# Optimization experiments

Measured on AMD Instinct MI355X. Metric: run time of the kernel, lower is better.

The kernel has to match this reference:

```python
import jax, jax.numpy as jnp
import numpy as np

N, FIN, F, H = 4096, 128, 64, 8
NEG = -1e10


def setup_inputs() -> dict:
    key = jax.random.key(0)
    ks = jax.random.split(key, 6)
    X = jax.random.normal(ks[0], (N, FIN), dtype=jnp.float32)
    # sparse-ish binary adjacency with self loops, stored dense (as the layer expects)
    A = (jax.random.uniform(ks[1], (N, N)) < 0.05).astype(jnp.int32)
    A = A.at[jnp.arange(N), jnp.arange(N)].set(1)
    W = jax.random.normal(ks[2], (H, FIN, F), dtype=jnp.float32) * (1.0 / np.sqrt(FIN))
    b = jnp.zeros((H, F), dtype=jnp.float32)
    a_self = jax.random.normal(ks[3], (H, F), dtype=jnp.float32) * (1.0 / np.sqrt(F))
    a_neigh = jax.random.normal(ks[4], (H, F), dtype=jnp.float32) * (1.0 / np.sqrt(F))
    return {"X": X, "A": A, "W": W, "b": b, "a_self": a_self, "a_neigh": a_neigh}


def reference(X, A, W, b, a_self, a_neigh):
    # Dropout layers run in inference mode in the original call -> identity.
    feats = jnp.einsum('nf,hfo->hno', X, W)              # [H, N, F]
    s_self = jnp.einsum('hno,ho->hn', feats, a_self)     # [H, N]
    s_neigh = jnp.einsum('hno,ho->hn', feats, a_neigh)   # [H, N]
    scores = s_self[:, :, None] + s_neigh[:, None, :]    # [H, N, N]
    scores = jnp.where(scores > 0, scores, 0.2 * scores)  # LeakyReLU(0.2)
    mask = (1.0 - A.astype(jnp.float32)) * NEG            # [N, N]
    attn = jax.nn.softmax(scores + mask[None], axis=-1)   # [H, N, N]
    out = jnp.einsum('hnm,hmo->hno', attn, feats) + b[:, None, :]
    out = jax.nn.elu(out)                                 # [H, N, F]
    # concat heads -> [N, H*F]
    return jnp.transpose(out, (1, 0, 2)).reshape(N, H * F)
```

## Files before the change

### kernel.cpp

```cpp
#include <hip/hip_runtime.h>
#include <cmath>


#define NN 4096
#define FIN 128
#define FF 64
#define HH 8

typedef _Float16 h2 __attribute__((ext_vector_type(2)));
typedef _Float16 h4 __attribute__((ext_vector_type(4)));
typedef _Float16 h8 __attribute__((ext_vector_type(8)));
typedef float f32x2 __attribute__((ext_vector_type(2)));
typedef float f32x4 __attribute__((ext_vector_type(4)));

union H8 {
  h8 v;
  h2 p[4];
};
union H4 {
  h4 v;
  h2 p[2];
};

static __device__ __forceinline__ float dot2acc(h2 a, float c) {
#if __has_builtin(__builtin_amdgcn_fdot2)
  return __builtin_amdgcn_fdot2(a, (h2){(_Float16)1.f, (_Float16)1.f}, c,
                                false);
#else
  return c + (float)a[0] + (float)a[1];
#endif
}

__global__ __launch_bounds__(256) void pack_kernel(
    const int* __restrict__ A, const float* __restrict__ W,
    unsigned long long* __restrict__ bits, _Float16* __restrict__ Wt16) {
  const int b = blockIdx.x;
  const int tid = threadIdx.x;
  if (b < NN) {
    const int wave = tid >> 6, lane = tid & 63;
    const int* ar = A + (size_t)b * NN;
#pragma unroll
    for (int g = 0; g < 4; ++g) {
      const int w0 = wave * 16 + g * 4;
      int v0 = ar[(w0 + 0) * 64 + lane];
      int v1 = ar[(w0 + 1) * 64 + lane];
      int v2 = ar[(w0 + 2) * 64 + lane];
      int v3 = ar[(w0 + 3) * 64 + lane];
      unsigned long long m0 = __ballot(v0 != 0);
      unsigned long long m1 = __ballot(v1 != 0);
      unsigned long long m2 = __ballot(v2 != 0);
      unsigned long long m3 = __ballot(v3 != 0);
      if (lane == 0) {
        bits[(b << 6) + w0 + 0] = m0;
        bits[(b << 6) + w0 + 1] = m1;
        bits[(b << 6) + w0 + 2] = m2;
        bits[(b << 6) + w0 + 3] = m3;
      }
    }
  } else {
    const int h0 = (b - NN) * 4;
    for (int h = h0; h < h0 + 4; ++h) {
      for (int idx = tid; idx < FIN * (FF / 4); idx += 256) {
        int k = idx >> 4, f4 = (idx & 15) << 2;
        f32x4 w = *(const f32x4*)(W + ((size_t)(h * FIN + k)) * FF + f4);
#pragma unroll
        for (int j = 0; j < 4; ++j)
          Wt16[((size_t)(h * FF + f4 + j)) * FIN + k] = (_Float16)w[j];
      }
    }
  }
}

__global__ __launch_bounds__(256) void feats_kernel(
    const float* __restrict__ X, const _Float16* __restrict__ Wt16,
    const float* __restrict__ a_self, const float* __restrict__ a_neigh,
    _Float16* __restrict__ feats_sw, _Float16* __restrict__ es_h,
    _Float16* __restrict__ esn_h, _Float16* __restrict__ et_h,
    _Float16* __restrict__ etn_h) {
  const int h = blockIdx.y;
  const int tid = threadIdx.x, wave = tid >> 6, lane = tid & 63;
  const int l16 = lane & 15, quad = lane >> 4;
  const int r0 = blockIdx.x * 64 + wave * 16;

  f32x4 acc[4];
#pragma unroll
  for (int nb = 0; nb < 4; ++nb) acc[nb] = (f32x4){0.f, 0.f, 0.f, 0.f};

  const float* xr = X + (size_t)(r0 + l16) * FIN;
  const _Float16* wb = Wt16 + (size_t)h * FF * FIN;
#pragma unroll
  for (int kt = 0; kt < 4; ++kt) {
    const int kof = kt * 32 + quad * 8;
    f32x4 x0 = *(const f32x4*)(xr + kof);
    f32x4 x1 = *(const f32x4*)(xr + kof + 4);
    h8 Af = {(_Float16)x0[0], (_Float16)x0[1], (_Float16)x0[2],
             (_Float16)x0[3], (_Float16)x1[0], (_Float16)x1[1],
             (_Float16)x1[2], (_Float16)x1[3]};
#pragma unroll
    for (int nb = 0; nb < 4; ++nb) {
      h8 Bf = *(const h8*)(wb + (size_t)(nb * 16 + l16) * FIN + kof);
      acc[nb] = __builtin_amdgcn_mfma_f32_16x16x32_f16(Af, Bf, acc[nb], 0, 0, 0);
    }
  }

  float as[4], an[4];
#pragma unroll
  for (int nb = 0; nb < 4; ++nb) {
    as[nb] = a_self[h * FF + nb * 16 + l16];
    an[nb] = a_neigh[h * FF + nb * 16 + l16];
  }
#pragma unroll
  for (int r = 0; r < 4; ++r) {
    float ps = acc[0][r] * as[0] + acc[1][r] * as[1] + acc[2][r] * as[2] +
               acc[3][r] * as[3];
    float pn = acc[0][r] * an[0] + acc[1][r] * an[1] + acc[2][r] * an[2] +
               acc[3][r] * an[3];
#pragma unroll
    for (int m = 1; m <= 8; m <<= 1) {
      ps += __shfl_xor(ps, m, 64);
      pn += __shfl_xor(pn, m, 64);
    }
    if (l16 == 0) {
      int node = h * NN + r0 + quad * 4 + r;
      es_h[node] = (_Float16)__expf(ps - 2.0f);
      esn_h[node] = (_Float16)__expf(0.2f * ps - 2.0f);
      et_h[node] = (_Float16)__expf(pn - 2.0f);
      etn_h[node] = (_Float16)__expf(0.2f * pn - 2.0f);
    }
  }

  const int kb = r0 >> 5;
  const int quadA = ((r0 >> 4) & 1) * 2 + (quad >> 1);
  const int jbase = (quad & 1) << 2;
#pragma unroll
  for (int nb = 0; nb < 4; ++nb) {
    h4 v = {(_Float16)acc[nb][0], (_Float16)acc[nb][1], (_Float16)acc[nb][2],
            (_Float16)acc[nb][3]};
    size_t off = ((size_t)((h * 128 + kb) * 4 + nb) << 9) +
                 ((quadA * 16 + l16) << 3) + jbase;
    *(h4*)(feats_sw + off) = v;
  }
}

__global__ __launch_bounds__(512, 4) void attn_kernel(
    const unsigned long long* __restrict__ Abits,
    const _Float16* __restrict__ feats_sw, const _Float16* __restrict__ es_h,
    const _Float16* __restrict__ esn_h, const _Float16* __restrict__ et_h,
    const _Float16* __restrict__ etn_h, const float* __restrict__ bias,
    float* __restrict__ out) {
  const int bid = blockIdx.x;
  const int h = bid & 7, n0 = (bid >> 3) << 6;
  const int tid = threadIdx.x, wave = tid >> 6, lane = tid & 63;
  const int l16 = lane & 15, quad = lane >> 4;

  __shared__ h4 lut16[16];
  __shared__ float accL[8][16][66];
  __shared__ float denL[8][64];
  if (tid < 16) {
    h4 m;
#pragma unroll
    for (int j = 0; j < 4; ++j) m[j] = (_Float16)((tid >> j) & 1);
    lut16[tid] = m;
  }
  __syncthreads();

  h2 esp[4], esnp[4];
#pragma unroll
  for (int rg = 0; rg < 4; ++rg) {
    _Float16 e = es_h[h * NN + n0 + rg * 16 + l16];
    _Float16 en = esn_h[h * NN + n0 + rg * 16 + l16];
    esp[rg] = (h2){e, e};
    esnp[rg] = (h2){en, en};
  }

  f32x4 acc[4][4];
  float dsA[4] = {0.f, 0.f, 0.f, 0.f}, dsB[4] = {0.f, 0.f, 0.f, 0.f};
#pragma unroll
  for (int rg = 0; rg < 4; ++rg)
#pragma unroll
    for (int nb = 0; nb < 4; ++nb) acc[rg][nb] = (f32x4){0.f, 0.f, 0.f, 0.f};

  const uint2* ab = (const uint2*)Abits;
  const int rowbase = n0 + l16;
  const _Float16* etp = et_h + h * NN + (quad << 3);
  const _Float16* etnp = etn_h + h * NN + (quad << 3);
  const _Float16* fb = feats_sw + ((size_t)h << 18) + (lane << 3);

  for (int ct = wave; ct < 64; ct += 8) {
    uint2 bits[4];
#pragma unroll
    for (int rg = 0; rg < 4; ++rg)
      bits[rg] = ab[((rowbase + rg * 16) << 6) + ct];
    const _Float16* fbt = fb + (ct << 12);
#pragma unroll
    for (int kf = 0; kf < 2; ++kf) {
      H8 ET, ETN;
      ET.v = *(const h8*)(etp + (ct << 6) + kf * 32);
      ETN.v = *(const h8*)(etnp + (ct << 6) + kf * 32);
      const _Float16* fk = fbt + (kf << 11);
      h8 B0 = *(const h8*)(fk);
      h8 B1 = *(const h8*)(fk + 512);
      h8 B2 = *(const h8*)(fk + 1024);
      h8 B3 = *(const h8*)(fk + 1536);
#pragma unroll
      for (int rg = 0; rg < 4; ++rg) {
        unsigned word = kf ? bits[rg].y : bits[rg].x;
        unsigned byt = (word >> (quad << 3)) & 0xFFu;
        H4 mlo, mhi;
        mlo.v = lut16[byt & 15u];
        mhi.v = lut16[byt >> 4];
        H8 P;
#pragma unroll
        for (int p = 0; p < 4; ++p) {
          h2 a = esp[rg] * ET.p[p];
          h2 b = esnp[rg] * ETN.p[p];
          h2 r = __builtin_elementwise_max(a, b);
          h2 pm = r * (p < 2 ? mlo.p[p] : mhi.p[p - 2]);
          P.p[p] = pm;
          if (p & 1)
            dsB[rg] = dot2acc(pm, dsB[rg]);
          else
            dsA[rg] = dot2acc(pm, dsA[rg]);
        }
        acc[rg][0] =
            __builtin_amdgcn_mfma_f32_16x16x32_f16(P.v, B0, acc[rg][0], 0, 0, 0);
        acc[rg][1] =
            __builtin_amdgcn_mfma_f32_16x16x32_f16(P.v, B1, acc[rg][1], 0, 0, 0);
        acc[rg][2] =
            __builtin_amdgcn_mfma_f32_16x16x32_f16(P.v, B2, acc[rg][2], 0, 0, 0);
        acc[rg][3] =
            __builtin_amdgcn_mfma_f32_16x16x32_f16(P.v, B3, acc[rg][3], 0, 0, 0);
      }
    }
  }

#pragma unroll
  for (int rg = 0; rg < 4; ++rg) {
    float d = dsA[rg] + dsB[rg];
    d += __shfl_xor(d, 16, 64);
    d += __shfl_xor(d, 32, 64);
    if (quad == 0) denL[wave][rg * 16 + l16] = d;
  }

  const int erow = tid >> 5, ec0 = (tid & 31) << 1;
#pragma unroll
  for (int ph = 0; ph < 4; ++ph) {
    __syncthreads();
#pragma unroll
    for (int nb = 0; nb < 4; ++nb)
#pragma unroll
      for (int r = 0; r < 4; ++r)
        accL[wave][quad * 4 + r][nb * 16 + l16] = acc[ph][nb][r];
    __syncthreads();
    const int grow = ph * 16 + erow;
    float dn = 0.f;
#pragma unroll
    for (int w = 0; w < 8; ++w) dn += denL[w][grow];
    float inv = 1.0f / dn;
    f32x2 v = (f32x2){0.f, 0.f};
#pragma unroll
    for (int w = 0; w < 8; ++w) v += *(const f32x2*)&accL[w][erow][ec0];
    const f32x2 bv = *(const f32x2*)(bias + h * FF + ec0);
#pragma unroll
    for (int i = 0; i < 2; ++i) {
      float x = v[i] * inv + bv[i];
      v[i] = x > 0.f ? x : (__expf(x) - 1.0f);
    }
    *(f32x2*)(out + (size_t)(n0 + grow) * (HH * FF) + h * FF + ec0) = v;
  }
}

extern "C" void kernel_launch(void* const* d_in, const int* in_sizes, int n_in,
                              void* d_out, int out_size, void* d_ws,
                              size_t ws_size, hipStream_t stream) {
  const float* X = (const float*)d_in[0];
  const int* A = (const int*)d_in[1];
  const float* W = (const float*)d_in[2];
  const float* b = (const float*)d_in[3];
  const float* a_self = (const float*)d_in[4];
  const float* a_neigh = (const float*)d_in[5];
  float* out = (float*)d_out;

  char* ws = (char*)d_ws;
  unsigned long long* Abits = (unsigned long long*)ws;
  _Float16* feats_sw = (_Float16*)(ws + (2u << 20));
  _Float16* es_h = (_Float16*)(ws + (6u << 20));
  _Float16* esn_h = (_Float16*)(ws + (6u << 20) + (64u << 10));
  _Float16* et_h = (_Float16*)(ws + (6u << 20) + (128u << 10));
  _Float16* etn_h = (_Float16*)(ws + (6u << 20) + (192u << 10));
  _Float16* Wt16 = (_Float16*)(ws + (6u << 20) + (256u << 10));

  pack_kernel<<<NN + 2, 256, 0, stream>>>(A, W, Abits, Wt16);
  feats_kernel<<<dim3(64, 8), 256, 0, stream>>>(X, Wt16, a_self, a_neigh,
                                                feats_sw, es_h, esn_h, et_h,
                                                etn_h);
  attn_kernel<<<512, 512, 0, stream>>>(Abits, feats_sw, es_h, esn_h, et_h,
                                       etn_h, b, out);
}
```

Before: 164.1 us.

## Pre-swizzle X and W into MFMA fragment layout and vectorize adjacency packing

The pack kernel now reads the adjacency matrix with 16-byte vector loads, transposes it through LDS so each lane holds the element matching the original ballot layout, and writes the bitmask words in pairs. It also converts W and X to fp16 directly into the MFMA fragment order, so the feats kernel does fully coalesced h8 loads with no per-call conversion or strided access. This removes redundant X conversion across the 8 heads and strided W reads, at the cost of 64 extra blocks, workspace for Xsw, and an LDS round-trip in packing.

```diff
diff --git a/kernel.cpp b/kernel.cpp
--- a/kernel.cpp
+++ b/kernel.cpp
@@ -33,46 +33,73 @@
 
 __global__ __launch_bounds__(256) void pack_kernel(
     const int* __restrict__ A, const float* __restrict__ W,
-    unsigned long long* __restrict__ bits, _Float16* __restrict__ Wt16) {
+    const float* __restrict__ X, unsigned long long* __restrict__ bits,
+    _Float16* __restrict__ Wsw, _Float16* __restrict__ Xsw) {
   const int b = blockIdx.x;
   const int tid = threadIdx.x;
+  const int wave = tid >> 6, lane = tid & 63;
   if (b < NN) {
-    const int wave = tid >> 6, lane = tid & 63;
+    __shared__ int ldsT[4][4][256];
     const int* ar = A + (size_t)b * NN;
-#pragma unroll
-    for (int g = 0; g < 4; ++g) {
-      const int w0 = wave * 16 + g * 4;
-      int v0 = ar[(w0 + 0) * 64 + lane];
-      int v1 = ar[(w0 + 1) * 64 + lane];
-      int v2 = ar[(w0 + 2) * 64 + lane];
-      int v3 = ar[(w0 + 3) * 64 + lane];
-      unsigned long long m0 = __ballot(v0 != 0);
-      unsigned long long m1 = __ballot(v1 != 0);
-      unsigned long long m2 = __ballot(v2 != 0);
-      unsigned long long m3 = __ballot(v3 != 0);
+    int4 v[4];
+#pragma unroll
+    for (int it = 0; it < 4; ++it) {
+      const int g = wave * 4 + it;
+      v[it] = *(const int4*)(ar + g * 256 + lane * 4);
+    }
+#pragma unroll
+    for (int it = 0; it < 4; ++it) *(int4*)&ldsT[wave][it][lane * 4] = v[it];
+    unsigned long long* br = bits + ((size_t)b << 6);
+#pragma unroll
+    for (int it = 0; it < 4; ++it) {
+      const int g = wave * 4 + it;
+      int w0 = ldsT[wave][it][0 * 64 + lane];
+      int w1 = ldsT[wave][it][1 * 64 + lane];
+      int w2 = ldsT[wave][it][2 * 64 + lane];
+      int w3 = ldsT[wave][it][3 * 64 + lane];
+      unsigned long long m0 = __ballot(w0 != 0);
+      unsigned long long m1 = __ballot(w1 != 0);
+      unsigned long long m2 = __ballot(w2 != 0);
+      unsigned long long m3 = __ballot(w3 != 0);
       if (lane == 0) {
-        bits[(b << 6) + w0 + 0] = m0;
-        bits[(b << 6) + w0 + 1] = m1;
-        bits[(b << 6) + w0 + 2] = m2;
-        bits[(b << 6) + w0 + 3] = m3;
+        ulonglong2 p0 = {m0, m1}, p1 = {m2, m3};
+        *(ulonglong2*)(br + g * 4 + 0) = p0;
+        *(ulonglong2*)(br + g * 4 + 2) = p1;
       }
     }
-  } else {
+  } else if (b < NN + 2) {
     const int h0 = (b - NN) * 4;
     for (int h = h0; h < h0 + 4; ++h) {
-      for (int idx = tid; idx < FIN * (FF / 4); idx += 256) {
-        int k = idx >> 4, f4 = (idx & 15) << 2;
-        f32x4 w = *(const f32x4*)(W + ((size_t)(h * FIN + k)) * FF + f4);
-#pragma unroll
-        for (int j = 0; j < 4; ++j)
-          Wt16[((size_t)(h * FF + f4 + j)) * FIN + k] = (_Float16)w[j];
+      for (int c = tid; c < 1024; c += 256) {
+        int ln = c & 63, nb = (c >> 6) & 3, kt = c >> 8;
+        int f = nb * 16 + (ln & 15);
+        int k0 = kt * 32 + (ln >> 4) * 8;
+        h8 v;
+#pragma unroll
+        for (int j = 0; j < 8; ++j)
+          v[j] = (_Float16)W[((size_t)(h * FIN) + k0 + j) * FF + f];
+        *(h8*)(Wsw + ((size_t)(((h * 4 + kt) * 4 + nb) * 64 + ln)) * 8) = v;
       }
     }
+  } else {
+    const int tile = (b - NN - 2) * 4 + wave;
+    const int l16 = lane & 15, quad = lane >> 4;
+    const float* xr = X + (size_t)(tile * 16 + l16) * FIN;
+#pragma unroll
+    for (int kt = 0; kt < 4; ++kt) {
+      int k0 = kt * 32 + quad * 8;
+      f32x4 x0 = *(const f32x4*)(xr + k0);
+      f32x4 x1 = *(const f32x4*)(xr + k0 + 4);
+      h8 v = {(_Float16)x0[0], (_Float16)x0[1], (_Float16)x0[2],
+              (_Float16)x0[3], (_Float16)x1[0], (_Float16)x1[1],
+              (_Float16)x1[2], (_Float16)x1[3]};
+      *(h8*)(Xsw + ((size_t)((tile * 4 + kt) * 64 + lane)) * 8) = v;
+    }
   }
 }
 
 __global__ __launch_bounds__(256) void feats_kernel(
-    const float* __restrict__ X, const _Float16* __restrict__ Wt16,
+    const _Float16* __restrict__ Xsw, const _Float16* __restrict__ Wsw,
     const float* __restrict__ a_self, const float* __restrict__ a_neigh,
     _Float16* __restrict__ feats_sw, _Float16* __restrict__ es_h,
     _Float16* __restrict__ esn_h, _Float16* __restrict__ et_h,
@@ -80,28 +107,25 @@
   const int h = blockIdx.y;
   const int tid = threadIdx.x, wave = tid >> 6, lane = tid & 63;
   const int l16 = lane & 15, quad = lane >> 4;
-  const int r0 = blockIdx.x * 64 + wave * 16;
+  const int rt = blockIdx.x * 4 + wave;
+  const int r0 = rt * 16;
 
   f32x4 acc[4];
 #pragma unroll
   for (int nb = 0; nb < 4; ++nb) acc[nb] = (f32x4){0.f, 0.f, 0.f, 0.f};
 
-  const float* xr = X + (size_t)(r0 + l16) * FIN;
-  const _Float16* wb = Wt16 + (size_t)h * FF * FIN;
-#pragma unroll
-  for (int kt = 0; kt < 4; ++kt) {
-    const int kof = kt * 32 + quad * 8;
-    f32x4 x0 = *(const f32x4*)(xr + kof);
-    f32x4 x1 = *(const f32x4*)(xr + kof + 4);
-    h8 Af = {(_Float16)x0[0], (_Float16)x0[1], (_Float16)x0[2],
-             (_Float16)x0[3], (_Float16)x1[0], (_Float16)x1[1],
-             (_Float16)x1[2], (_Float16)x1[3]};
+  const _Float16* xp = Xsw + ((size_t)(rt * 4) * 64 + lane) * 8;
+  const _Float16* wp = Wsw + ((size_t)(h * 16) * 64 + lane) * 8;
+  h8 Af[4];
+#pragma unroll
+  for (int kt = 0; kt < 4; ++kt) Af[kt] = *(const h8*)(xp + kt * 512);
+#pragma unroll
+  for (int kt = 0; kt < 4; ++kt)
 #pragma unroll
     for (int nb = 0; nb < 4; ++nb) {
-      h8 Bf = *(const h8*)(wb + (size_t)(nb * 16 + l16) * FIN + kof);
-      acc[nb] = __builtin_amdgcn_mfma_f32_16x16x32_f16(Af, Bf, acc[nb], 0, 0, 0);
-    }
-  }
+      h8 Bf = *(const h8*)(wp + (kt * 4 + nb) * 512);
+      acc[nb] = __builtin_amdgcn_mfma_f32_16x16x32_f16(Af[kt], Bf, acc[nb], 0, 0, 0);
+    }
 
   float as[4], an[4];
 #pragma unroll
@@ -288,10 +312,11 @@
   _Float16* esn_h = (_Float16*)(ws + (6u << 20) + (64u << 10));
   _Float16* et_h = (_Float16*)(ws + (6u << 20) + (128u << 10));
   _Float16* etn_h = (_Float16*)(ws + (6u << 20) + (192u << 10));
-  _Float16* Wt16 = (_Float16*)(ws + (6u << 20) + (256u << 10));
-
-  pack_kernel<<<NN + 2, 256, 0, stream>>>(A, W, Abits, Wt16);
-  feats_kernel<<<dim3(64, 8), 256, 0, stream>>>(X, Wt16, a_self, a_neigh,
+  _Float16* Wsw = (_Float16*)(ws + (6u << 20) + (256u << 10));
+  _Float16* Xsw = (_Float16*)(ws + (6u << 20) + (384u << 10));
+
+  pack_kernel<<<NN + 66, 256, 0, stream>>>(A, W, X, Abits, Wsw, Xsw);
+  feats_kernel<<<dim3(64, 8), 256, 0, stream>>>(Xsw, Wsw, a_self, a_neigh,
                                                 feats_sw, es_h, esn_h, et_h,
                                                 etn_h);
   attn_kernel<<<512, 512, 0, stream>>>(Abits, feats_sw, es_h, esn_h, et_h,
```

New measurement: 145.4 us. 11.3% less time.
